# Kernel tuning notes

Hardware: AMD Instinct MI355X
Metric: run time of the kernel (lower is better)

Reference implementation:

```python
import jax, jax.numpy as jnp
import numpy as np

EMBED_DIM = 512
NUM_HEADS = 8
NUM_RULES = 16
HEAD_DIM = EMBED_DIM // NUM_HEADS


def setup_inputs() -> dict:
    key = jax.random.key(0)
    ks = jax.random.split(key, 10)
    B, S, E, H, R, D = 4, 2048, EMBED_DIM, NUM_HEADS, NUM_RULES, HEAD_DIM
    lim_q = 1.0 / np.sqrt(E)
    lim_v = 1.0 / np.sqrt(E)
    return {
        "query": jax.random.normal(ks[0], (B, S, E), jnp.float32),
        "key": jax.random.normal(ks[1], (B, S, E), jnp.float32),
        "value": jax.random.normal(ks[2], (B, S, E), jnp.float32),
        "Wq": jax.random.uniform(ks[3], (E, E), jnp.float32, -lim_q, lim_q),
        "bq": jax.random.uniform(ks[4], (E,), jnp.float32, -lim_q, lim_q),
        "Wv": jax.random.uniform(ks[5], (E * R, E), jnp.float32, -lim_v, lim_v),
        "bv": jax.random.uniform(ks[6], (E * R,), jnp.float32, -lim_v, lim_v),
        "Wo": jax.random.uniform(ks[7], (E, E), jnp.float32, -lim_q, lim_q),
        "bo": jax.random.uniform(ks[8], (E,), jnp.float32, -lim_q, lim_q),
        "rules_keys": 0.02 * jax.random.normal(ks[9], (H, R, D), jnp.float32),
        "rules_widths": jnp.ones((H, R, D), jnp.float32),
    }


def reference(query, key, value, Wq, bq, Wv, bv, Wo, bo, rules_keys, rules_widths):
    B, S, E = query.shape
    H, R, D = NUM_HEADS, NUM_RULES, HEAD_DIM
    scale = D ** -0.5
    # preprocessing_query: Linear + scale, split heads -> (b, h, s, d)
    q = (query @ Wq.T + bq) * scale
    q = q.reshape(B, S, H, D).transpose(0, 2, 1, 3)
    # custom_distance (l1): |q - rule_key| broadcast over rules -> (b, h, s, r, d)
    diff = jnp.abs(q[:, :, :, None, :] - rules_keys[None, :, None, :, :])
    # get_z_values: z = mean_d( -0.5 * (diff / width)^2 ) -> (b, h, s, r)
    z = -0.5 * jnp.mean(jnp.square(diff / rules_widths[None, :, None, :, :]), axis=-1)
    # softmax over rules (last dim), dropout is identity (p=0)
    attn = jax.nn.softmax(z, axis=-1)  # (b, h, s, r)
    # preprocessing_value: Linear(E -> E*R) + scale, 'b s (h d r) -> b s h d r'
    v = (value @ Wv.T + bv) * scale
    v = v.reshape(B, S, H, D, R)
    # Fnn_output = attn * v summed over rules -> (b, s, h, d)
    out = jnp.einsum("bhsr,bshdr->bshd", attn, v)
    # torch: (b,s,h,d).transpose(1,2).contiguous().view(b, -1, h*d)
    out = out.transpose(0, 2, 1, 3).reshape(B, -1, H * D)
    return out @ Wo.T + bo
```

## Files before the change

### kernel.cpp

```cpp
#include <hip/hip_runtime.h>
#include <stdint.h>

#define TOKENS 8192
#define EDIM 512
#define HNUM 8
#define RNUM 16
#define DDIM 64
#define KDIM 512

typedef short v8s __attribute__((ext_vector_type(8)));
typedef float v4f __attribute__((ext_vector_type(4)));

__device__ inline float b2f(unsigned short u) {
    union { unsigned int i; float f; } c; c.i = ((unsigned int)u) << 16; return c.f;
}
__device__ inline unsigned short f2b(float f) {
    union { float f; unsigned int i; } c; c.f = f;
    unsigned int i = c.i + 0x7fffu + ((c.i >> 16) & 1u);
    return (unsigned short)(i >> 16);
}

#define GLD16(dst, src) \
    __builtin_amdgcn_global_load_lds((__attribute__((address_space(1))) void*)(src), \
                                     (__attribute__((address_space(3))) void*)(dst), 16, 0, 0)

__global__ __launch_bounds__(256)
void cvt5(const float* __restrict__ s0, const float* __restrict__ s1,
          const float* __restrict__ s2, const float* __restrict__ s3,
          const float* __restrict__ s4,
          unsigned short* __restrict__ d0, unsigned short* __restrict__ d1,
          unsigned short* __restrict__ d2, unsigned short* __restrict__ d3,
          unsigned short* __restrict__ d4,
          int n0, int n1, int n2, int n3, int n4)
{
    const float* s; unsigned short* d; int n;
    switch (blockIdx.y) {
        case 0: s = s0; d = d0; n = n0; break;
        case 1: s = s1; d = d1; n = n1; break;
        case 2: s = s2; d = d2; n = n2; break;
        case 3: s = s3; d = d3; n = n3; break;
        default: s = s4; d = d4; n = n4; break;
    }
    size_t base = (size_t)blockIdx.x * 2048 + (size_t)threadIdx.x * 8;
    if (base >= (size_t)n) return;
    const float4* sp = (const float4*)(s + base);
    float4 f0 = sp[0], f1 = sp[1];
    v8s o;
    o[0] = (short)f2b(f0.x); o[1] = (short)f2b(f0.y);
    o[2] = (short)f2b(f0.z); o[3] = (short)f2b(f0.w);
    o[4] = (short)f2b(f1.x); o[5] = (short)f2b(f1.y);
    o[6] = (short)f2b(f1.z); o[7] = (short)f2b(f1.w);
    *(v8s*)(d + base) = o;
}

template <int MODE>
__global__ __launch_bounds__(256, 4)
void gemm64(const unsigned short* __restrict__ A,
            const unsigned short* __restrict__ B,
            const float* __restrict__ bias,
            float* __restrict__ outF,
            unsigned short* __restrict__ outH)
{
    __shared__ unsigned short As[64 * 32];
    __shared__ unsigned short Bs[64 * 32];

    const int tid  = threadIdx.x;
    const int w    = tid >> 6;
    const int lane = tid & 63;
    const int quad = lane >> 4;
    const int l16  = lane & 15;
    const int wm   = w >> 1, wn = w & 1;
    const int m0   = blockIdx.x * 64;
    const int n0   = blockIdx.y * 64;

    v4f acc[2][2];
#pragma unroll
    for (int i = 0; i < 2; ++i)
#pragma unroll
        for (int j = 0; j < 2; ++j)
            acc[i][j] = (v4f){0.f, 0.f, 0.f, 0.f};

    for (int kt = 0; kt < KDIM / 32; ++kt) {
        int c = w * 64 + lane;
        const unsigned short* sa = A + (size_t)(m0 + (c >> 2)) * KDIM + kt * 32 + (c & 3) * 8;
        GLD16(&As[w * 512], sa);
        const unsigned short* sb = B + (size_t)(n0 + (c >> 2)) * KDIM + kt * 32 + (c & 3) * 8;
        GLD16(&Bs[w * 512], sb);
        __syncthreads();

        v8s af[2], bf[2];
#pragma unroll
        for (int mt = 0; mt < 2; ++mt)
            af[mt] = *(const v8s*)&As[(wm * 32 + mt * 16 + l16) * 32 + quad * 8];
#pragma unroll
        for (int nt = 0; nt < 2; ++nt)
            bf[nt] = *(const v8s*)&Bs[(wn * 32 + nt * 16 + l16) * 32 + quad * 8];
#pragma unroll
        for (int mt = 0; mt < 2; ++mt)
#pragma unroll
            for (int nt = 0; nt < 2; ++nt)
                acc[mt][nt] = __builtin_amdgcn_mfma_f32_16x16x32_bf16(af[mt], bf[nt], acc[mt][nt], 0, 0, 0);
        __syncthreads();
    }

#pragma unroll
    for (int mt = 0; mt < 2; ++mt)
#pragma unroll
        for (int nt = 0; nt < 2; ++nt) {
            int col = n0 + wn * 32 + nt * 16 + l16;
            float bb = bias[col];
#pragma unroll
            for (int rg = 0; rg < 4; ++rg) {
                int row = m0 + wm * 32 + mt * 16 + quad * 4 + rg;
                float v = acc[mt][nt][rg] + bb;
                if (MODE == 0) outH[(size_t)row * EDIM + col] = f2b(v * 0.125f);
                else           outF[(size_t)row * EDIM + col] = v;
            }
        }
}

__global__ __launch_bounds__(256, 2)
void gemm_v(const unsigned short* __restrict__ A,
            const unsigned short* __restrict__ B,
            const float* __restrict__ bias,
            unsigned short* __restrict__ outH,
            const float* __restrict__ attn)
{
    __shared__ unsigned short As[128 * 32];
    __shared__ unsigned short Bs[128 * 32];
    __shared__ unsigned short Os[128 * 8];

    const int tid  = threadIdx.x;
    const int w    = tid >> 6;
    const int lane = tid & 63;
    const int quad = lane >> 4;
    const int l16  = lane & 15;
    const int wm   = w >> 1, wn = w & 1;
    const int m0   = blockIdx.x * 128;
    const int n0   = blockIdx.y * 128;

    v4f acc[4][4];
#pragma unroll
    for (int i = 0; i < 4; ++i)
#pragma unroll
        for (int j = 0; j < 4; ++j)
            acc[i][j] = (v4f){0.f, 0.f, 0.f, 0.f};

    for (int kt = 0; kt < KDIM / 32; ++kt) {
#pragma unroll
        for (int p = 0; p < 2; ++p) {
            int cb = w * 128 + p * 64;
            int c  = cb + lane;
            const unsigned short* sa = A + (size_t)(m0 + (c >> 2)) * KDIM + kt * 32 + (c & 3) * 8;
            GLD16(&As[cb * 8], sa);
            const unsigned short* sb = B + (size_t)(n0 + (c >> 2)) * KDIM + kt * 32 + (c & 3) * 8;
            GLD16(&Bs[cb * 8], sb);
        }
        __syncthreads();

        v8s af[4], bf[4];
#pragma unroll
        for (int mt = 0; mt < 4; ++mt)
            af[mt] = *(const v8s*)&As[(wm * 64 + mt * 16 + l16) * 32 + quad * 8];
#pragma unroll
        for (int nt = 0; nt < 4; ++nt)
            bf[nt] = *(const v8s*)&Bs[(wn * 64 + nt * 16 + l16) * 32 + quad * 8];
#pragma unroll
        for (int mt = 0; mt < 4; ++mt)
#pragma unroll
            for (int nt = 0; nt < 4; ++nt)
                acc[mt][nt] = __builtin_amdgcn_mfma_f32_16x16x32_bf16(af[mt], bf[nt], acc[mt][nt], 0, 0, 0);
        __syncthreads();
    }

    const int h  = m0 >> 10;
    const int d0 = (m0 >> 4) & 63;
    float4 bias4[4];
#pragma unroll
    for (int mt = 0; mt < 4; ++mt)
        bias4[mt] = *(const float4*)&bias[m0 + wm * 64 + mt * 16 + quad * 4];
#pragma unroll
    for (int nt = 0; nt < 4; ++nt) {
        int token = n0 + wn * 64 + nt * 16 + l16;
        float4 av = *(const float4*)&attn[(size_t)token * (HNUM * RNUM) + h * RNUM + quad * 4];
#pragma unroll
        for (int mt = 0; mt < 4; ++mt) {
            v4f a = acc[mt][nt];
            float val = (a[0] + bias4[mt].x) * av.x
                      + (a[1] + bias4[mt].y) * av.y
                      + (a[2] + bias4[mt].z) * av.z
                      + (a[3] + bias4[mt].w) * av.w;
            val += __shfl_xor(val, 16);
            val += __shfl_xor(val, 32);
            if (quad == 0)
                Os[(wn * 64 + nt * 16 + l16) * 8 + (wm * 4 + mt)] = f2b(val * 0.125f);
        }
    }
    __syncthreads();
    if (tid < 128) {
        int sg = n0 + tid;
        int g  = (sg >> 11) * 2048 + h * 256 + ((sg & 2047) >> 3);
        int j  = (sg & 7) * 64 + d0;
        *(v8s*)&outH[(size_t)g * EDIM + j] = *(const v8s*)&Os[tid * 8];
    }
}

#define RST 72
__global__ __launch_bounds__(256)
void rules_softmax(const unsigned short* __restrict__ q,
                   const float* __restrict__ rk,
                   const float* __restrict__ rw,
                   float* __restrict__ attn)
{
    __shared__ float ql[16 * RST];
    __shared__ float rkl[16 * RST];
    __shared__ float iwl[16 * RST];
    const int h   = blockIdx.y;
    const int t0  = blockIdx.x * 16;
    const int tid = threadIdx.x;

#pragma unroll
    for (int i = 0; i < 4; ++i) {
        int jj = tid + i * 256;
        int r = jj >> 6, d = jj & 63;
        rkl[r * RST + d] = rk[h * (RNUM * DDIM) + jj];
        float wv = rw[h * (RNUM * DDIM) + jj];
        iwl[r * RST + d] = 1.0f / (wv * wv);
    }
    {
        int jj = tid * 4;
        int row = jj >> 6, d = jj & 63;
        const unsigned short* src = q + (size_t)(t0 + row) * EDIM + h * DDIM + d;
        unsigned short u0 = src[0], u1 = src[1], u2 = src[2], u3 = src[3];
        ql[row * RST + d + 0] = b2f(u0);
        ql[row * RST + d + 1] = b2f(u1);
        ql[row * RST + d + 2] = b2f(u2);
        ql[row * RST + d + 3] = b2f(u3);
    }
    __syncthreads();

    const int tl = tid >> 4;
    const int r  = tid & 15;
    const float* qrow = &ql[tl * RST];
    const float* krow = &rkl[r * RST];
    const float* wrow = &iwl[r * RST];
    float z = 0.f;
#pragma unroll
    for (int d4 = 0; d4 < 16; ++d4) {
        float4 qv = *(const float4*)&qrow[d4 * 4];
        float4 kv = *(const float4*)&krow[d4 * 4];
        float4 wv = *(const float4*)&wrow[d4 * 4];
        float a0 = qv.x - kv.x; z += a0 * a0 * wv.x;
        float a1 = qv.y - kv.y; z += a1 * a1 * wv.y;
        float a2 = qv.z - kv.z; z += a2 * a2 * wv.z;
        float a3 = qv.w - kv.w; z += a3 * a3 * wv.w;
    }
    z *= (-0.5f / 64.f);
    float mx = z;
#pragma unroll
    for (int s = 1; s < 16; s <<= 1) mx = fmaxf(mx, __shfl_xor(mx, s));
    float e = __expf(z - mx);
    float sum = e;
#pragma unroll
    for (int s = 1; s < 16; s <<= 1) sum += __shfl_xor(sum, s);
    attn[(size_t)(t0 + tl) * (HNUM * RNUM) + h * RNUM + r] = e / sum;
}

extern "C" void kernel_launch(void* const* d_in, const int* in_sizes, int n_in,
                              void* d_out, int out_size, void* d_ws, size_t ws_size,
                              hipStream_t stream) {
    const float* query = (const float*)d_in[0];
    const float* value = (const float*)d_in[2];
    const float* Wq = (const float*)d_in[3];
    const float* bq = (const float*)d_in[4];
    const float* Wv = (const float*)d_in[5];
    const float* bv = (const float*)d_in[6];
    const float* Wo = (const float*)d_in[7];
    const float* bo = (const float*)d_in[8];
    const float* rk = (const float*)d_in[9];
    const float* rw = (const float*)d_in[10];

    char* ws = (char*)d_ws;
    unsigned short* qbf  = (unsigned short*)(ws);
    unsigned short* vbf  = (unsigned short*)(ws + (size_t)( 8 << 20));
    unsigned short* Wqb  = (unsigned short*)(ws + (size_t)(16 << 20));
    unsigned short* Wvb  = (unsigned short*)(ws + (size_t)(17 << 20));
    unsigned short* Wob  = (unsigned short*)(ws + (size_t)(25 << 20));
    unsigned short* out1 = (unsigned short*)(ws + (size_t)(26 << 20));
    unsigned short* qf   = (unsigned short*)(ws + (size_t)(34 << 20));
    float* attn          = (float*)(ws + (size_t)(42 << 20));

    dim3 blk(256);
    cvt5<<<dim3(2048, 5), blk, 0, stream>>>(query, value, Wv, Wq, Wo,
                                            qbf, vbf, Wvb, Wqb, Wob,
                                            TOKENS * EDIM, TOKENS * EDIM, EDIM * RNUM * EDIM,
                                            EDIM * EDIM, EDIM * EDIM);
    gemm64<0><<<dim3(TOKENS / 64, EDIM / 64), blk, 0, stream>>>(qbf, Wqb, bq, nullptr, qf);
    rules_softmax<<<dim3(TOKENS / 16, HNUM), blk, 0, stream>>>(qf, rk, rw, attn);
    gemm_v<<<dim3((EDIM * RNUM) / 128, TOKENS / 128), blk, 0, stream>>>(Wvb, vbf, bv, out1, attn);
    gemm64<2><<<dim3(TOKENS / 64, EDIM / 64), blk, 0, stream>>>(out1, Wob, bo, (float*)d_out, nullptr);
}
```

Measured before the change: 233.7 us.

## Rewrite value GEMM as 256x256 double-buffered, swizzled, 8-wave pipelined kernel

The dominant value-projection GEMM now uses 256x256 tiles with 512 threads, a K-step of 64, XOR-swizzled LDS layout and double-buffered async global-to-LDS loads. Loads for the next stages are interleaved with MFMA quadrants under explicit barriers and wait counts, with raised priority during MFMA bursts. The 1D grid is remapped for locality. The aim is to raise data reuse, hide global latency and avoid bank conflicts. In exchange it uses far more LDS and registers, which may limit occupancy.

```diff
diff --git a/kernel.cpp b/kernel.cpp
--- a/kernel.cpp
+++ b/kernel.cpp
@@ -119,89 +119,154 @@
         }
 }
 
-__global__ __launch_bounds__(256, 2)
+__device__ __forceinline__ v8s ldfrag(const unsigned short* base, int r, int g) {
+    return *(const v8s*)(base + (r << 6) + ((g ^ (r & 7)) << 3));
+}
+
+#define SCHED0 __builtin_amdgcn_sched_barrier(0)
+#define BARX do { SCHED0; __builtin_amdgcn_s_barrier(); SCHED0; } while (0)
+#define LGKM0 do { asm volatile("s_waitcnt lgkmcnt(0)" ::: "memory"); SCHED0; } while (0)
+#define WAITV(n) do { asm volatile("s_waitcnt vmcnt(" #n ")" ::: "memory"); SCHED0; } while (0)
+
+#define STAGE_H(ldsArr, bufi, half_, gptr, rowbase, ktv) do { \
+    const unsigned short* s_ = (gptr) + (size_t)((rowbase) + (half_) * 128 + (w << 4) + rsub) * KDIM \
+                               + (ktv) * 64 + (gsw << 3); \
+    GLD16(&ldsArr[bufi][(half_) * 8192 + (w << 10)], s_); \
+    GLD16(&ldsArr[bufi][(half_) * 8192 + (w << 10) + 512], s_ + 8 * KDIM); \
+} while (0)
+
+#define LDA8(mq_) do { \
+    _Pragma("unroll") \
+    for (int mi = 0; mi < 4; ++mi) \
+        _Pragma("unroll") \
+        for (int ks = 0; ks < 2; ++ks) \
+            af[mi * 2 + ks] = ldfrag(abase, wm * 64 + (mq_) * 128 + mi * 16 + l16, ks * 4 + quad); \
+} while (0)
+
+#define LDB4(nq_) do { \
+    _Pragma("unroll") \
+    for (int ni = 0; ni < 2; ++ni) \
+        _Pragma("unroll") \
+        for (int ks = 0; ks < 2; ++ks) \
+            bf[ni * 2 + ks] = ldfrag(bbase, wn * 32 + (nq_) * 128 + ni * 16 + l16, ks * 4 + quad); \
+} while (0)
+
+#define MFMA16(mq_, nq_) do { \
+    _Pragma("unroll") \
+    for (int ks = 0; ks < 2; ++ks) \
+        _Pragma("unroll") \
+        for (int mi = 0; mi < 4; ++mi) \
+            _Pragma("unroll") \
+            for (int ni = 0; ni < 2; ++ni) \
+                acc[(mq_) * 2 + (nq_)][mi][ni] = __builtin_amdgcn_mfma_f32_16x16x32_bf16( \
+                    af[mi * 2 + ks], bf[ni * 2 + ks], acc[(mq_) * 2 + (nq_)][mi][ni], 0, 0, 0); \
+} while (0)
+
+__global__ __launch_bounds__(512, 2)
 void gemm_v(const unsigned short* __restrict__ A,
             const unsigned short* __restrict__ B,
             const float* __restrict__ bias,
             unsigned short* __restrict__ outH,
             const float* __restrict__ attn)
 {
-    __shared__ unsigned short As[128 * 32];
-    __shared__ unsigned short Bs[128 * 32];
-    __shared__ unsigned short Os[128 * 8];
+    __shared__ unsigned short As[2][16384];
+    __shared__ unsigned short Bs[2][16384];
 
     const int tid  = threadIdx.x;
     const int w    = tid >> 6;
     const int lane = tid & 63;
     const int quad = lane >> 4;
     const int l16  = lane & 15;
-    const int wm   = w >> 1, wn = w & 1;
-    const int m0   = blockIdx.x * 128;
-    const int n0   = blockIdx.y * 128;
-
-    v4f acc[4][4];
-#pragma unroll
-    for (int i = 0; i < 4; ++i)
-#pragma unroll
-        for (int j = 0; j < 4; ++j)
-            acc[i][j] = (v4f){0.f, 0.f, 0.f, 0.f};
-
-    for (int kt = 0; kt < KDIM / 32; ++kt) {
-#pragma unroll
-        for (int p = 0; p < 2; ++p) {
-            int cb = w * 128 + p * 64;
-            int c  = cb + lane;
-            const unsigned short* sa = A + (size_t)(m0 + (c >> 2)) * KDIM + kt * 32 + (c & 3) * 8;
-            GLD16(&As[cb * 8], sa);
-            const unsigned short* sb = B + (size_t)(n0 + (c >> 2)) * KDIM + kt * 32 + (c & 3) * 8;
-            GLD16(&Bs[cb * 8], sb);
-        }
-        __syncthreads();
-
-        v8s af[4], bf[4];
-#pragma unroll
-        for (int mt = 0; mt < 4; ++mt)
-            af[mt] = *(const v8s*)&As[(wm * 64 + mt * 16 + l16) * 32 + quad * 8];
-#pragma unroll
-        for (int nt = 0; nt < 4; ++nt)
-            bf[nt] = *(const v8s*)&Bs[(wn * 64 + nt * 16 + l16) * 32 + quad * 8];
-#pragma unroll
-        for (int mt = 0; mt < 4; ++mt)
-#pragma unroll
-            for (int nt = 0; nt < 4; ++nt)
-                acc[mt][nt] = __builtin_amdgcn_mfma_f32_16x16x32_bf16(af[mt], bf[nt], acc[mt][nt], 0, 0, 0);
-        __syncthreads();
-    }
-
+    const int wm   = w >> 2;
+    const int wn   = w & 3;
+    const int rsub = lane >> 3;
+    const int gsw  = (lane & 7) ^ rsub;
+
+    const int id = ((blockIdx.x & 7) << 7) | (blockIdx.x >> 3);
+    const int m0 = (id & 31) << 8;
+    const int n0 = (id >> 5) << 8;
+
+    v4f acc[4][4][2];
+#pragma unroll
+    for (int q = 0; q < 4; ++q)
+#pragma unroll
+        for (int mi = 0; mi < 4; ++mi)
+#pragma unroll
+            for (int ni = 0; ni < 2; ++ni)
+                acc[q][mi][ni] = (v4f){0.f, 0.f, 0.f, 0.f};
+
+    v8s af[8], bf[4];
+
+    STAGE_H(As, 0, 0, A, m0, 0);
+    STAGE_H(Bs, 0, 1, B, n0, 0);
+    STAGE_H(As, 0, 1, A, m0, 0);
+    STAGE_H(Bs, 0, 0, B, n0, 0);
+    STAGE_H(As, 1, 0, A, m0, 1);
+    STAGE_H(Bs, 1, 1, B, n0, 1);
+    WAITV(4);
+    BARX;
+
+    for (int T = 0; T < KDIM / 64; ++T) {
+        const unsigned short* abase = &As[T & 1][0];
+        const unsigned short* bbase = &Bs[T & 1][0];
+        const int bn_ = (T & 1) ^ 1;
+
+        LDA8(0); LDB4(0);
+        if (T + 1 < 8) STAGE_H(As, bn_, 1, A, m0, T + 1);
+        BARX; LGKM0;
+        __builtin_amdgcn_s_setprio(1); MFMA16(0, 0); __builtin_amdgcn_s_setprio(0);
+        BARX;
+
+        LDB4(1);
+        if (T + 1 < 8) STAGE_H(Bs, bn_, 0, B, n0, T + 1);
+        BARX; LGKM0;
+        __builtin_amdgcn_s_setprio(1); MFMA16(0, 1); __builtin_amdgcn_s_setprio(0);
+        BARX;
+
+        LDA8(1);
+        if (T + 2 < 8) STAGE_H(As, T & 1, 0, A, m0, T + 2);
+        BARX; LGKM0;
+        __builtin_amdgcn_s_setprio(1); MFMA16(1, 1); __builtin_amdgcn_s_setprio(0);
+        BARX;
+
+        LDB4(0);
+        if (T + 2 < 8) STAGE_H(Bs, T & 1, 1, B, n0, T + 2);
+        BARX; LGKM0;
+        __builtin_amdgcn_s_setprio(1); MFMA16(1, 0); __builtin_amdgcn_s_setprio(0);
+        if (T < 6) { WAITV(4); } else { WAITV(0); }
+        BARX;
+    }
+
+    unsigned short* Osp = &As[0][0];
     const int h  = m0 >> 10;
     const int d0 = (m0 >> 4) & 63;
-    float4 bias4[4];
-#pragma unroll
-    for (int mt = 0; mt < 4; ++mt)
-        bias4[mt] = *(const float4*)&bias[m0 + wm * 64 + mt * 16 + quad * 4];
-#pragma unroll
-    for (int nt = 0; nt < 4; ++nt) {
-        int token = n0 + wn * 64 + nt * 16 + l16;
-        float4 av = *(const float4*)&attn[(size_t)token * (HNUM * RNUM) + h * RNUM + quad * 4];
-#pragma unroll
-        for (int mt = 0; mt < 4; ++mt) {
-            v4f a = acc[mt][nt];
-            float val = (a[0] + bias4[mt].x) * av.x
-                      + (a[1] + bias4[mt].y) * av.y
-                      + (a[2] + bias4[mt].z) * av.z
-                      + (a[3] + bias4[mt].w) * av.w;
-            val += __shfl_xor(val, 16);
-            val += __shfl_xor(val, 32);
-            if (quad == 0)
-                Os[(wn * 64 + nt * 16 + l16) * 8 + (wm * 4 + mt)] = f2b(val * 0.125f);
-        }
-    }
+#pragma unroll
+    for (int mq = 0; mq < 2; ++mq)
+#pragma unroll
+        for (int nq = 0; nq < 2; ++nq)
+#pragma unroll
+            for (int mi = 0; mi < 4; ++mi) {
+                float4 bias4 = *(const float4*)&bias[m0 + mq * 128 + wm * 64 + mi * 16 + quad * 4];
+#pragma unroll
+                for (int ni = 0; ni < 2; ++ni) {
+                    int tloc  = nq * 128 + wn * 32 + ni * 16 + l16;
+                    float4 av = *(const float4*)&attn[(size_t)(n0 + tloc) * (HNUM * RNUM) + h * RNUM + quad * 4];
+                    v4f a = acc[mq * 2 + nq][mi][ni];
+                    float val = (a[0] + bias4.x) * av.x + (a[1] + bias4.y) * av.y
+                              + (a[2] + bias4.z) * av.z + (a[3] + bias4.w) * av.w;
+                    val += __shfl_xor(val, 16);
+                    val += __shfl_xor(val, 32);
+                    if (quad == 0)
+                        Osp[tloc * 16 + (mq * 8 + wm * 4 + mi)] = f2b(val * 0.125f);
+                }
+            }
     __syncthreads();
-    if (tid < 128) {
-        int sg = n0 + tid;
+    {
+        int tl = tid >> 1, hf = tid & 1;
+        int sg = n0 + tl;
         int g  = (sg >> 11) * 2048 + h * 256 + ((sg & 2047) >> 3);
-        int j  = (sg & 7) * 64 + d0;
-        *(v8s*)&outH[(size_t)g * EDIM + j] = *(const v8s*)&Os[tid * 8];
+        int j  = (sg & 7) * 64 + d0 + hf * 8;
+        *(v8s*)&outH[(size_t)g * EDIM + j] = *(const v8s*)&Osp[tl * 16 + hf * 8];
     }
 }
 
@@ -297,6 +362,6 @@
                                             EDIM * EDIM, EDIM * EDIM);
     gemm64<0><<<dim3(TOKENS / 64, EDIM / 64), blk, 0, stream>>>(qbf, Wqb, bq, nullptr, qf);
     rules_softmax<<<dim3(TOKENS / 16, HNUM), blk, 0, stream>>>(qf, rk, rw, attn);
-    gemm_v<<<dim3((EDIM * RNUM) / 128, TOKENS / 128), blk, 0, stream>>>(Wvb, vbf, bv, out1, attn);
+    gemm_v<<<dim3(1024), dim3(512), 0, stream>>>(Wvb, vbf, bv, out1, attn);
     gemm64<2><<<dim3(TOKENS / 64, EDIM / 64), blk, 0, stream>>>(out1, Wob, bo, (float*)d_out, nullptr);
 }
```

Result: slower. 245.2 us (+4.9%).
